# Kernel tuning notes

Hardware: AMD Instinct MI355X
Metric: run time of the kernel (lower is better)

The kernel has to match this reference:

```python
import jax, jax.numpy as jnp
import numpy as np

B, Q, K = 4, 128, 1024
DQ, DK, DV, H = 512, 512, 512, 256
NEG_INF = -1e6


def setup_inputs() -> dict:
    key = jax.random.key(0)
    ks = jax.random.split(key, 6)
    queries = jax.random.normal(ks[0], (B, Q, DQ), dtype=jnp.float32)
    keys = jax.random.normal(ks[1], (B, K, DK), dtype=jnp.float32)
    values = jax.random.normal(ks[2], (B, K, DV), dtype=jnp.float32)
    valid_lens = jax.random.randint(ks[3], (B,), 1, K + 1, dtype=jnp.int32)
    # Learned params (Dense use_bias=False): W_q [DQ,H], W_k [DK,H], w_v [H] (Dense(1) squeezed)
    Wq = jax.random.normal(ks[4], (DQ, H), dtype=jnp.float32) / np.sqrt(DQ)
    Wk = jax.random.normal(ks[5], (DK, H), dtype=jnp.float32) / np.sqrt(DK)
    wv = jax.random.normal(jax.random.fold_in(key, 7), (H,), dtype=jnp.float32) / np.sqrt(H)
    return {"queries": queries, "keys": keys, "values": values,
            "valid_lens": valid_lens, "Wq": Wq, "Wk": Wk, "wv": wv}


def reference(queries, keys, values, valid_lens, Wq, Wk, wv):
    q = queries @ Wq                       # [B,Q,H]
    k = keys @ Wk                          # [B,K,H]
    feats = jnp.tanh(q[:, :, None, :] + k[:, None, :, :])   # [B,Q,K,H]
    scores = jnp.einsum('bqkh,h->bqk', feats, wv)            # [B,Q,K]
    mask = jnp.arange(scores.shape[-1]) < valid_lens[:, None, None]  # [B,1,K]
    scores = jnp.where(mask, scores, NEG_INF)
    attn = jax.nn.softmax(scores, axis=-1)                   # [B,Q,K]
    # dropout is identity at inference
    return attn @ values                                     # [B,Q,DV]
```

## Files before the change

kernel.cpp:

```cpp
#include <hip/hip_runtime.h>

#define Bn 4
#define Qn 128
#define Kn 1024
#define Dn 512
#define Hn 256

__device__ __forceinline__ float fast_tanh(float x) {
    float e = __expf(2.0f * x);
    return 1.0f - 2.0f * __builtin_amdgcn_rcpf(1.0f + e);
}

#define PBK 64

__global__ __launch_bounds__(512, 4) void proj_kernel(
    const float* __restrict__ queries, const float* __restrict__ keys,
    const float* __restrict__ Wq, const float* __restrict__ Wk,
    const int* __restrict__ valid_lens,
    float* __restrict__ proj0, float* __restrict__ proj1)
{
    const int blk = blockIdx.x;
    const int kc = blk & 1;
    const int nt = (blk >> 1) & 3;
    const int mt = blk >> 3;
    const int t = threadIdx.x;
    const float* Asrc; const float* W;
    int m0, drow;
    if (mt < 8) {
        m0 = mt * 64;
        drow = m0;
        Asrc = queries; W = Wq;
    } else {
        int r0 = (mt - 8) * 64;
        int b = r0 >> 10;
        if ((r0 & 1023) >= valid_lens[b]) return;
        m0 = r0;
        drow = 512 + r0;
        Asrc = keys; W = Wk;
    }
    const int n0 = nt * 64;
    const int k0 = kc * 256;
    float* Dst = (kc ? proj1 : proj0) + (size_t)drow * Hn;

    __shared__ float s_a[PBK][68];
    __shared__ float s_b[PBK][64];

    const int tt   = t & 255;
    const int kh   = t >> 8;
    const int trow = tt >> 4;
    const int tcol = tt & 15;
    const int kklo = kh << 5;

    const int lrow = t >> 4;
    const int lc4  = t & 15;

    float acc[4][4] = {{0.f}};
    float4 ra[2], rb[2];

    #pragma unroll
    for (int i = 0; i < 2; ++i) {
        ra[i] = *(const float4*)(Asrc + (size_t)(m0 + lrow + i * 32) * Dn + k0 + lc4 * 4);
        rb[i] = *(const float4*)(W + (size_t)(k0 + lrow + i * 32) * Hn + n0 + lc4 * 4);
    }

    for (int kt = 0; kt < 4; ++kt) {
        __syncthreads();
        #pragma unroll
        for (int i = 0; i < 2; ++i) {
            int row = lrow + i * 32;
            s_a[lc4 * 4 + 0][row] = ra[i].x;
            s_a[lc4 * 4 + 1][row] = ra[i].y;
            s_a[lc4 * 4 + 2][row] = ra[i].z;
            s_a[lc4 * 4 + 3][row] = ra[i].w;
            *(float4*)&s_b[row][lc4 * 4] = rb[i];
        }
        __syncthreads();
        if (kt < 3) {
            const int d0n = k0 + (kt + 1) * PBK;
            #pragma unroll
            for (int i = 0; i < 2; ++i) {
                ra[i] = *(const float4*)(Asrc + (size_t)(m0 + lrow + i * 32) * Dn + d0n + lc4 * 4);
                rb[i] = *(const float4*)(W + (size_t)(d0n + lrow + i * 32) * Hn + n0 + lc4 * 4);
            }
        }
        #pragma unroll
        for (int kk = 0; kk < 32; ++kk) {
            float4 a4 = *(const float4*)&s_a[kklo + kk][trow * 4];
            float4 b4 = *(const float4*)&s_b[kklo + kk][tcol * 4];
            float a[4] = {a4.x, a4.y, a4.z, a4.w};
            float b[4] = {b4.x, b4.y, b4.z, b4.w};
            #pragma unroll
            for (int i = 0; i < 4; ++i)
                #pragma unroll
                for (int j = 0; j < 4; ++j)
                    acc[i][j] += a[i] * b[j];
        }
    }

    __syncthreads();
    float* red = &s_a[0][0];
    if (kh) {
        #pragma unroll
        for (int i = 0; i < 4; ++i)
            #pragma unroll
            for (int j = 0; j < 4; ++j)
                red[tt * 17 + i * 4 + j] = acc[i][j];
    }
    __syncthreads();
    if (!kh) {
        #pragma unroll
        for (int i = 0; i < 4; ++i) {
            float4 o;
            o.x = acc[i][0] + red[tt * 17 + i * 4 + 0];
            o.y = acc[i][1] + red[tt * 17 + i * 4 + 1];
            o.z = acc[i][2] + red[tt * 17 + i * 4 + 2];
            o.w = acc[i][3] + red[tt * 17 + i * 4 + 3];
            *(float4*)(Dst + (size_t)(trow * 4 + i) * Hn + n0 + tcol * 4) = o;
        }
    }
}

#define SK_KT 16
#define SK_PAD 260

__global__ __launch_bounds__(256) void score_kernel(
    const float* __restrict__ proj0, const float* __restrict__ proj1,
    const float* __restrict__ wv, const int* __restrict__ valid_lens,
    float* __restrict__ escores, float* __restrict__ rowsum)
{
    const int blk = blockIdx.x;
    const int kt = blk & 63;
    const int qt = (blk >> 6) & 31;
    const int b  = blk >> 11;
    const int vlen = valid_lens[b];
    const int k0 = kt * SK_KT;
    if (k0 >= vlen) return;
    const int q0 = qt * 4;
    const int t = threadIdx.x;

    __shared__ float s_k[SK_KT * SK_PAD];
    __shared__ float s_q[4 * Hn];
    __shared__ float s_wv[Hn];

    {
        const float4* k0p = reinterpret_cast<const float4*>(
            proj0 + ((size_t)512 + (size_t)b * Kn + k0) * Hn);
        const float4* k1p = reinterpret_cast<const float4*>(
            proj1 + ((size_t)512 + (size_t)b * Kn + k0) * Hn);
        #pragma unroll
        for (int i = 0; i < 4; ++i) {
            int idx = t + i * 256;
            int row = idx >> 6, c4 = idx & 63;
            float4 a = k0p[idx];
            float4 c = k1p[idx];
            a.x += c.x; a.y += c.y; a.z += c.z; a.w += c.w;
            *reinterpret_cast<float4*>(&s_k[row * SK_PAD + c4 * 4]) = a;
        }
        float4 qa = reinterpret_cast<const float4*>(
            proj0 + ((size_t)b * Qn + q0) * Hn)[t];
        float4 qb = reinterpret_cast<const float4*>(
            proj1 + ((size_t)b * Qn + q0) * Hn)[t];
        qa.x += qb.x; qa.y += qb.y; qa.z += qb.z; qa.w += qb.w;
        reinterpret_cast<float4*>(s_q)[t] = qa;
        if (t < 64)
            reinterpret_cast<float4*>(s_wv)[t] =
                reinterpret_cast<const float4*>(wv)[t];
    }
    __syncthreads();

    const int wave = t >> 6;
    const int lane = t & 63;
    const int kloc = lane & 15;
    const int hq   = lane >> 4;

    const float4* kr = reinterpret_cast<const float4*>(&s_k[kloc * SK_PAD + hq * 64]);
    const float4* qr = reinterpret_cast<const float4*>(&s_q[wave * Hn + hq * 64]);
    const float4* wr = reinterpret_cast<const float4*>(&s_wv[hq * 64]);

    float s = 0.0f;
    #pragma unroll
    for (int i = 0; i < 16; ++i) {
        float4 kv = kr[i];
        float4 qv = qr[i];
        float4 wq = wr[i];
        s += wq.x * fast_tanh(qv.x + kv.x);
        s += wq.y * fast_tanh(qv.y + kv.y);
        s += wq.z * fast_tanh(qv.z + kv.z);
        s += wq.w * fast_tanh(qv.w + kv.w);
    }
    s += __shfl_xor(s, 16, 64);
    s += __shfl_xor(s, 32, 64);

    const int k = k0 + kloc;
    float e = 0.0f;
    if (lane < 16 && k < vlen) {
        e = __expf(s);
        escores[((size_t)b * Qn + q0 + wave) * Kn + k] = e;
    }
    #pragma unroll
    for (int off = 32; off; off >>= 1)
        e += __shfl_xor(e, off, 64);
    if (lane == 0)
        atomicAdd(&rowsum[b * Qn + q0 + wave], e);
}

__global__ __launch_bounds__(256) void av_kernel(
    const float* __restrict__ escores, const float* __restrict__ values,
    const float* __restrict__ rowsum, float* __restrict__ out)
{
    const int blk = blockIdx.x;
    const int kc = blk & 3;
    const int dh = (blk >> 2) & 1;
    const int qt = (blk >> 3) & 15;
    const int b  = blk >> 7;
    const int t = threadIdx.x;
    const int q0 = qt * 8;
    const int kb = kc * 256;
    const int d  = dh * 256 + t;

    __shared__ float s_e[8][256];
    #pragma unroll
    for (int i = 0; i < 2; ++i) {
        int idx = t + i * 256;
        int row = idx >> 6, c4 = idx & 63;
        *(float4*)&s_e[row][c4 * 4] = *(const float4*)(
            escores + ((size_t)(b * Qn + q0 + row)) * Kn + kb + c4 * 4);
    }
    __syncthreads();

    const float* vb = values + ((size_t)b * Kn + kb) * Dn + d;
    float acc[8] = {0.f};
    #pragma unroll 2
    for (int k = 0; k < 256; k += 4) {
        float v0 = vb[(size_t)(k + 0) * Dn];
        float v1 = vb[(size_t)(k + 1) * Dn];
        float v2 = vb[(size_t)(k + 2) * Dn];
        float v3 = vb[(size_t)(k + 3) * Dn];
        #pragma unroll
        for (int j = 0; j < 8; ++j) {
            float4 e4 = *(const float4*)&s_e[j][k];
            acc[j] += e4.x * v0 + e4.y * v1 + e4.z * v2 + e4.w * v3;
        }
    }
    float* op = out + ((size_t)(b * Qn + q0)) * Dn + d;
    #pragma unroll
    for (int j = 0; j < 8; ++j) {
        float inv = __builtin_amdgcn_rcpf(rowsum[b * Qn + q0 + j]);
        atomicAdd(op + (size_t)j * Dn, acc[j] * inv);
    }
}

extern "C" void kernel_launch(void* const* d_in, const int* in_sizes, int n_in,
                              void* d_out, int out_size, void* d_ws, size_t ws_size,
                              hipStream_t stream) {
    const float* queries    = (const float*)d_in[0];
    const float* keys       = (const float*)d_in[1];
    const float* values     = (const float*)d_in[2];
    const int*   valid_lens = (const int*)  d_in[3];
    const float* Wq         = (const float*)d_in[4];
    const float* Wk         = (const float*)d_in[5];
    const float* wv         = (const float*)d_in[6];
    float* out = (float*)d_out;

    const size_t PROJ_F = (size_t)4608 * Hn;
    float* proj0   = (float*)d_ws;
    float* proj1   = proj0 + PROJ_F;
    float* escores = proj1 + PROJ_F;
    float* rowsum  = escores + (size_t)Bn * Qn * Kn;

    hipMemsetAsync(escores, 0, (size_t)(Bn * Qn * Kn + Bn * Qn) * sizeof(float),
                   stream);
    hipMemsetAsync(out, 0, (size_t)Bn * Qn * Dn * sizeof(float), stream);
    proj_kernel<<<576, 512, 0, stream>>>(queries, keys, Wq, Wk, valid_lens,
                                         proj0, proj1);
    score_kernel<<<Bn * 32 * 64, 256, 0, stream>>>(proj0, proj1, wv,
                                                   valid_lens, escores, rowsum);
    av_kernel<<<512, 256, 0, stream>>>(escores, values, rowsum, out);
}
```

Before: 153.4 us.

## Fuse projection, scoring and AV into one cooperative persistent kernel

Replaces the three kernels and two memsets with a single cooperative kernel of 256 blocks. Blocks zero the output and rowsum buffers themselves, run the projection GEMM as a loop over jobs, and separate the stages with grid-wide syncs. The score stage is retiled so each wave handles 8 query rows, which reuses each key tile across more queries. The AV stage now skips key chunks past valid_len. This removes launch and memset overhead and raises data reuse. In exchange it runs at lower parallelism (256 blocks), no longer skips projecting masked key rows, and the uneven job split across blocks may leave some blocks idle at each grid sync.

```diff
diff --git a/kernel.cpp b/kernel.cpp
--- a/kernel.cpp
+++ b/kernel.cpp
@@ -1,4 +1,7 @@
 #include <hip/hip_runtime.h>
+#include <hip/hip_cooperative_groups.h>
+
+namespace cg = cooperative_groups;
 
 #define Bn 4
 #define Qn 128
@@ -11,242 +14,238 @@
     return 1.0f - 2.0f * __builtin_amdgcn_rcpf(1.0f + e);
 }
 
-#define PBK 64
-
-__global__ __launch_bounds__(512, 4) void proj_kernel(
+__global__ __launch_bounds__(512) void fused_kernel(
     const float* __restrict__ queries, const float* __restrict__ keys,
+    const float* __restrict__ values, const int* __restrict__ valid_lens,
     const float* __restrict__ Wq, const float* __restrict__ Wk,
-    const int* __restrict__ valid_lens,
-    float* __restrict__ proj0, float* __restrict__ proj1)
+    const float* __restrict__ wv,
+    float* __restrict__ proj0, float* __restrict__ proj1,
+    float* __restrict__ escores, float* __restrict__ rowsum,
+    float* __restrict__ out)
 {
+    __shared__ float smem[20800];
+    const int t = threadIdx.x;
     const int blk = blockIdx.x;
-    const int kc = blk & 1;
-    const int nt = (blk >> 1) & 3;
-    const int mt = blk >> 3;
-    const int t = threadIdx.x;
-    const float* Asrc; const float* W;
-    int m0, drow;
-    if (mt < 8) {
-        m0 = mt * 64;
-        drow = m0;
-        Asrc = queries; W = Wq;
-    } else {
-        int r0 = (mt - 8) * 64;
-        int b = r0 >> 10;
-        if ((r0 & 1023) >= valid_lens[b]) return;
-        m0 = r0;
-        drow = 512 + r0;
-        Asrc = keys; W = Wk;
-    }
-    const int n0 = nt * 64;
-    const int k0 = kc * 256;
-    float* Dst = (kc ? proj1 : proj0) + (size_t)drow * Hn;
-
-    __shared__ float s_a[PBK][68];
-    __shared__ float s_b[PBK][64];
-
-    const int tt   = t & 255;
-    const int kh   = t >> 8;
-    const int trow = tt >> 4;
-    const int tcol = tt & 15;
-    const int kklo = kh << 5;
-
-    const int lrow = t >> 4;
-    const int lc4  = t & 15;
-
-    float acc[4][4] = {{0.f}};
-    float4 ra[2], rb[2];
-
-    #pragma unroll
-    for (int i = 0; i < 2; ++i) {
-        ra[i] = *(const float4*)(Asrc + (size_t)(m0 + lrow + i * 32) * Dn + k0 + lc4 * 4);
-        rb[i] = *(const float4*)(W + (size_t)(k0 + lrow + i * 32) * Hn + n0 + lc4 * 4);
-    }
-
-    for (int kt = 0; kt < 4; ++kt) {
-        __syncthreads();
-        #pragma unroll
-        for (int i = 0; i < 2; ++i) {
-            int row = lrow + i * 32;
-            s_a[lc4 * 4 + 0][row] = ra[i].x;
-            s_a[lc4 * 4 + 1][row] = ra[i].y;
-            s_a[lc4 * 4 + 2][row] = ra[i].z;
-            s_a[lc4 * 4 + 3][row] = ra[i].w;
-            *(float4*)&s_b[row][lc4 * 4] = rb[i];
+    cg::grid_group grid = cg::this_grid();
+
+    {
+        const int gid = blk * 512 + t;
+        float4 z = {0.f, 0.f, 0.f, 0.f};
+        if (gid < (Bn * Qn * Dn) / 4) ((float4*)out)[gid] = z;
+        if (gid < (Bn * Qn) / 4)      ((float4*)rowsum)[gid] = z;
+    }
+
+    {
+        float* s_a = smem;
+        float* s_b = smem + 64 * 68;
+        const int lrow = t >> 4, lc4 = t & 15;
+        const int tt = t & 255, kh = t >> 8;
+        const int trow = tt >> 4, tcol = tt & 15;
+        const int kklo = kh << 5;
+
+        for (int job = blk; job < 576; job += 256) {
+            const int kc = job & 1;
+            const int nt = (job >> 1) & 3;
+            const int mt = job >> 3;
+            const float *Asrc, *W; int m0, drow;
+            if (mt < 8) { m0 = mt * 64;       drow = m0;       Asrc = queries; W = Wq; }
+            else        { m0 = (mt - 8) * 64; drow = 512 + m0; Asrc = keys;    W = Wk; }
+            const int n0 = nt * 64;
+            const int kb = kc * 256;
+            float* Dst = (kc ? proj1 : proj0) + (size_t)drow * Hn;
+
+            float acc[4][4] = {{0.f}};
+            float4 ra[2], rb[2];
+            #pragma unroll
+            for (int i = 0; i < 2; ++i) {
+                ra[i] = *(const float4*)(Asrc + (size_t)(m0 + lrow + i * 32) * Dn + kb + lc4 * 4);
+                rb[i] = *(const float4*)(W + (size_t)(kb + lrow + i * 32) * Hn + n0 + lc4 * 4);
+            }
+            for (int kt = 0; kt < 4; ++kt) {
+                __syncthreads();
+                #pragma unroll
+                for (int i = 0; i < 2; ++i) {
+                    int row = lrow + i * 32;
+                    s_a[(lc4 * 4 + 0) * 68 + row] = ra[i].x;
+                    s_a[(lc4 * 4 + 1) * 68 + row] = ra[i].y;
+                    s_a[(lc4 * 4 + 2) * 68 + row] = ra[i].z;
+                    s_a[(lc4 * 4 + 3) * 68 + row] = ra[i].w;
+                    *(float4*)&s_b[row * 64 + lc4 * 4] = rb[i];
+                }
+                __syncthreads();
+                if (kt < 3) {
+                    const int d0n = kb + (kt + 1) * 64;
+                    #pragma unroll
+                    for (int i = 0; i < 2; ++i) {
+                        ra[i] = *(const float4*)(Asrc + (size_t)(m0 + lrow + i * 32) * Dn + d0n + lc4 * 4);
+                        rb[i] = *(const float4*)(W + (size_t)(d0n + lrow + i * 32) * Hn + n0 + lc4 * 4);
+                    }
+                }
+                #pragma unroll
+                for (int kk = 0; kk < 32; ++kk) {
+                    float4 a4 = *(const float4*)&s_a[(kklo + kk) * 68 + trow * 4];
+                    float4 b4 = *(const float4*)&s_b[(kklo + kk) * 64 + tcol * 4];
+                    float a[4] = {a4.x, a4.y, a4.z, a4.w};
+                    float b[4] = {b4.x, b4.y, b4.z, b4.w};
+                    #pragma unroll
+                    for (int i = 0; i < 4; ++i)
+                        #pragma unroll
+                        for (int j = 0; j < 4; ++j)
+                            acc[i][j] += a[i] * b[j];
+                }
+            }
+            __syncthreads();
+            float* red = smem;
+            if (kh) {
+                #pragma unroll
+                for (int i = 0; i < 4; ++i)
+                    #pragma unroll
+                    for (int j = 0; j < 4; ++j)
+                        red[tt * 17 + i * 4 + j] = acc[i][j];
+            }
+            __syncthreads();
+            if (!kh) {
+                #pragma unroll
+                for (int i = 0; i < 4; ++i) {
+                    float4 o;
+                    o.x = acc[i][0] + red[tt * 17 + i * 4 + 0];
+                    o.y = acc[i][1] + red[tt * 17 + i * 4 + 1];
+                    o.z = acc[i][2] + red[tt * 17 + i * 4 + 2];
+                    o.w = acc[i][3] + red[tt * 17 + i * 4 + 3];
+                    *(float4*)(Dst + (size_t)(trow * 4 + i) * Hn + n0 + tcol * 4) = o;
+                }
+            }
+            __syncthreads();
         }
-        __syncthreads();
-        if (kt < 3) {
-            const int d0n = k0 + (kt + 1) * PBK;
+    }
+
+    __threadfence();
+    grid.sync();
+    __threadfence();
+
+    {
+        float* s_k  = smem;
+        float* s_q  = smem + 16 * 260;
+        float* s_wv = smem + 16 * 260 + 64 * 256;
+        for (int job = blk; job < 512; job += 256) {
+            const int kt = job & 63;
+            const int qh = (job >> 6) & 1;
+            const int b  = job >> 7;
+            const int vlen = valid_lens[b];
+            const int k0 = kt * 16;
+            if (k0 >= vlen) continue;
+            const int q0 = qh * 64;
+
+            const float4* k0p = (const float4*)(proj0 + ((size_t)512 + b * Kn + k0) * Hn);
+            const float4* k1p = (const float4*)(proj1 + ((size_t)512 + b * Kn + k0) * Hn);
             #pragma unroll
             for (int i = 0; i < 2; ++i) {
-                ra[i] = *(const float4*)(Asrc + (size_t)(m0 + lrow + i * 32) * Dn + d0n + lc4 * 4);
-                rb[i] = *(const float4*)(W + (size_t)(d0n + lrow + i * 32) * Hn + n0 + lc4 * 4);
-            }
+                int idx = t + i * 512;
+                int row = idx >> 6, c4 = idx & 63;
+                float4 a = k0p[idx], c = k1p[idx];
+                a.x += c.x; a.y += c.y; a.z += c.z; a.w += c.w;
+                *(float4*)&s_k[row * 260 + c4 * 4] = a;
+            }
+            const float4* q0p = (const float4*)(proj0 + ((size_t)b * Qn + q0) * Hn);
+            const float4* q1p = (const float4*)(proj1 + ((size_t)b * Qn + q0) * Hn);
+            #pragma unroll
+            for (int i = 0; i < 8; ++i) {
+                int idx = t + i * 512;
+                float4 a = q0p[idx], c = q1p[idx];
+                a.x += c.x; a.y += c.y; a.z += c.z; a.w += c.w;
+                ((float4*)s_q)[idx] = a;
+            }
+            if (t < 64) ((float4*)s_wv)[t] = ((const float4*)wv)[t];
+            __syncthreads();
+
+            const int w = t >> 6, lane = t & 63;
+            const int kloc = lane & 15, hq = lane >> 4;
+            const float4* kr = (const float4*)&s_k[kloc * 260 + hq * 64];
+            const float4* wr = (const float4*)&s_wv[hq * 64];
+            const float*  qb = &s_q[(size_t)(w * 8) * 256 + hq * 64];
+            float acc[8] = {0.f, 0.f, 0.f, 0.f, 0.f, 0.f, 0.f, 0.f};
+            #pragma unroll 4
+            for (int i = 0; i < 16; ++i) {
+                float4 kv = kr[i];
+                float4 wq = wr[i];
+                #pragma unroll
+                for (int qr = 0; qr < 8; ++qr) {
+                    float4 qv = *(const float4*)&qb[qr * 256 + i * 4];
+                    acc[qr] += wq.x * fast_tanh(qv.x + kv.x)
+                             + wq.y * fast_tanh(qv.y + kv.y)
+                             + wq.z * fast_tanh(qv.z + kv.z)
+                             + wq.w * fast_tanh(qv.w + kv.w);
+                }
+            }
+            const int k = k0 + kloc;
+            #pragma unroll
+            for (int qr = 0; qr < 8; ++qr) {
+                float s = acc[qr];
+                s += __shfl_xor(s, 16, 64);
+                s += __shfl_xor(s, 32, 64);
+                float e = 0.f;
+                if (lane < 16 && k < vlen) {
+                    e = __expf(s);
+                    escores[((size_t)b * Qn + q0 + w * 8 + qr) * Kn + k] = e;
+                }
+                e += __shfl_xor(e, 8, 64);
+                e += __shfl_xor(e, 4, 64);
+                e += __shfl_xor(e, 2, 64);
+                e += __shfl_xor(e, 1, 64);
+                if (lane == 0)
+                    atomicAdd(&rowsum[b * Qn + q0 + w * 8 + qr], e);
+            }
+            __syncthreads();
         }
-        #pragma unroll
-        for (int kk = 0; kk < 32; ++kk) {
-            float4 a4 = *(const float4*)&s_a[kklo + kk][trow * 4];
-            float4 b4 = *(const float4*)&s_b[kklo + kk][tcol * 4];
-            float a[4] = {a4.x, a4.y, a4.z, a4.w};
-            float b[4] = {b4.x, b4.y, b4.z, b4.w};
-            #pragma unroll
-            for (int i = 0; i < 4; ++i)
-                #pragma unroll
-                for (int j = 0; j < 4; ++j)
-                    acc[i][j] += a[i] * b[j];
+    }
+
+    __threadfence();
+    grid.sync();
+    __threadfence();
+
+    {
+        float* s_e = smem;
+        const int kc = blk & 3;
+        const int qt = (blk >> 2) & 15;
+        const int b  = blk >> 6;
+        const int vlen = valid_lens[b];
+        const int kb = kc * 256;
+        if (kb < vlen) {
+            const int q0 = qt * 8;
+            const int row = t >> 6, c4 = t & 63;
+            {
+                const float* esrc = escores + ((size_t)b * Qn + q0 + row) * Kn + kb + c4 * 4;
+                const int kbase = kb + c4 * 4;
+                float4 ev;
+                ev.x = (kbase + 0 < vlen) ? esrc[0] : 0.f;
+                ev.y = (kbase + 1 < vlen) ? esrc[1] : 0.f;
+                ev.z = (kbase + 2 < vlen) ? esrc[2] : 0.f;
+                ev.w = (kbase + 3 < vlen) ? esrc[3] : 0.f;
+                *(float4*)&s_e[row * 256 + c4 * 4] = ev;
+            }
+            __syncthreads();
+            const int d = t;
+            const float* vb = values + ((size_t)b * Kn + kb) * Dn + d;
+            float acc[8] = {0.f, 0.f, 0.f, 0.f, 0.f, 0.f, 0.f, 0.f};
+            #pragma unroll 2
+            for (int k = 0; k < 256; k += 4) {
+                float v0 = vb[(size_t)(k + 0) * Dn];
+                float v1 = vb[(size_t)(k + 1) * Dn];
+                float v2 = vb[(size_t)(k + 2) * Dn];
+                float v3 = vb[(size_t)(k + 3) * Dn];
+                #pragma unroll
+                for (int j = 0; j < 8; ++j) {
+                    float4 e4 = *(const float4*)&s_e[j * 256 + k];
+                    acc[j] += e4.x * v0 + e4.y * v1 + e4.z * v2 + e4.w * v3;
+                }
+            }
+            float* op = out + ((size_t)b * Qn + q0) * Dn + d;
+            #pragma unroll
+            for (int j = 0; j < 8; ++j) {
+                float inv = __builtin_amdgcn_rcpf(rowsum[b * Qn + q0 + j]);
+                atomicAdd(op + (size_t)j * Dn, acc[j] * inv);
+            }
         }
-    }
-
-    __syncthreads();
-    float* red = &s_a[0][0];
-    if (kh) {
-        #pragma unroll
-        for (int i = 0; i < 4; ++i)
-            #pragma unroll
-            for (int j = 0; j < 4; ++j)
-                red[tt * 17 + i * 4 + j] = acc[i][j];
-    }
-    __syncthreads();
-    if (!kh) {
-        #pragma unroll
-        for (int i = 0; i < 4; ++i) {
-            float4 o;
-            o.x = acc[i][0] + red[tt * 17 + i * 4 + 0];
-            o.y = acc[i][1] + red[tt * 17 + i * 4 + 1];
-            o.z = acc[i][2] + red[tt * 17 + i * 4 + 2];
-            o.w = acc[i][3] + red[tt * 17 + i * 4 + 3];
-            *(float4*)(Dst + (size_t)(trow * 4 + i) * Hn + n0 + tcol * 4) = o;
-        }
-    }
-}
-
-#define SK_KT 16
-#define SK_PAD 260
-
-__global__ __launch_bounds__(256) void score_kernel(
-    const float* __restrict__ proj0, const float* __restrict__ proj1,
-    const float* __restrict__ wv, const int* __restrict__ valid_lens,
-    float* __restrict__ escores, float* __restrict__ rowsum)
-{
-    const int blk = blockIdx.x;
-    const int kt = blk & 63;
-    const int qt = (blk >> 6) & 31;
-    const int b  = blk >> 11;
-    const int vlen = valid_lens[b];
-    const int k0 = kt * SK_KT;
-    if (k0 >= vlen) return;
-    const int q0 = qt * 4;
-    const int t = threadIdx.x;
-
-    __shared__ float s_k[SK_KT * SK_PAD];
-    __shared__ float s_q[4 * Hn];
-    __shared__ float s_wv[Hn];
-
-    {
-        const float4* k0p = reinterpret_cast<const float4*>(
-            proj0 + ((size_t)512 + (size_t)b * Kn + k0) * Hn);
-        const float4* k1p = reinterpret_cast<const float4*>(
-            proj1 + ((size_t)512 + (size_t)b * Kn + k0) * Hn);
-        #pragma unroll
-        for (int i = 0; i < 4; ++i) {
-            int idx = t + i * 256;
-            int row = idx >> 6, c4 = idx & 63;
-            float4 a = k0p[idx];
-            float4 c = k1p[idx];
-            a.x += c.x; a.y += c.y; a.z += c.z; a.w += c.w;
-            *reinterpret_cast<float4*>(&s_k[row * SK_PAD + c4 * 4]) = a;
-        }
-        float4 qa = reinterpret_cast<const float4*>(
-            proj0 + ((size_t)b * Qn + q0) * Hn)[t];
-        float4 qb = reinterpret_cast<const float4*>(
-            proj1 + ((size_t)b * Qn + q0) * Hn)[t];
-        qa.x += qb.x; qa.y += qb.y; qa.z += qb.z; qa.w += qb.w;
-        reinterpret_cast<float4*>(s_q)[t] = qa;
-        if (t < 64)
-            reinterpret_cast<float4*>(s_wv)[t] =
-                reinterpret_cast<const float4*>(wv)[t];
-    }
-    __syncthreads();
-
-    const int wave = t >> 6;
-    const int lane = t & 63;
-    const int kloc = lane & 15;
-    const int hq   = lane >> 4;
-
-    const float4* kr = reinterpret_cast<const float4*>(&s_k[kloc * SK_PAD + hq * 64]);
-    const float4* qr = reinterpret_cast<const float4*>(&s_q[wave * Hn + hq * 64]);
-    const float4* wr = reinterpret_cast<const float4*>(&s_wv[hq * 64]);
-
-    float s = 0.0f;
-    #pragma unroll
-    for (int i = 0; i < 16; ++i) {
-        float4 kv = kr[i];
-        float4 qv = qr[i];
-        float4 wq = wr[i];
-        s += wq.x * fast_tanh(qv.x + kv.x);
-        s += wq.y * fast_tanh(qv.y + kv.y);
-        s += wq.z * fast_tanh(qv.z + kv.z);
-        s += wq.w * fast_tanh(qv.w + kv.w);
-    }
-    s += __shfl_xor(s, 16, 64);
-    s += __shfl_xor(s, 32, 64);
-
-    const int k = k0 + kloc;
-    float e = 0.0f;
-    if (lane < 16 && k < vlen) {
-        e = __expf(s);
-        escores[((size_t)b * Qn + q0 + wave) * Kn + k] = e;
-    }
-    #pragma unroll
-    for (int off = 32; off; off >>= 1)
-        e += __shfl_xor(e, off, 64);
-    if (lane == 0)
-        atomicAdd(&rowsum[b * Qn + q0 + wave], e);
-}
-
-__global__ __launch_bounds__(256) void av_kernel(
-    const float* __restrict__ escores, const float* __restrict__ values,
-    const float* __restrict__ rowsum, float* __restrict__ out)
-{
-    const int blk = blockIdx.x;
-    const int kc = blk & 3;
-    const int dh = (blk >> 2) & 1;
-    const int qt = (blk >> 3) & 15;
-    const int b  = blk >> 7;
-    const int t = threadIdx.x;
-    const int q0 = qt * 8;
-    const int kb = kc * 256;
-    const int d  = dh * 256 + t;
-
-    __shared__ float s_e[8][256];
-    #pragma unroll
-    for (int i = 0; i < 2; ++i) {
-        int idx = t + i * 256;
-        int row = idx >> 6, c4 = idx & 63;
-        *(float4*)&s_e[row][c4 * 4] = *(const float4*)(
-            escores + ((size_t)(b * Qn + q0 + row)) * Kn + kb + c4 * 4);
-    }
-    __syncthreads();
-
-    const float* vb = values + ((size_t)b * Kn + kb) * Dn + d;
-    float acc[8] = {0.f};
-    #pragma unroll 2
-    for (int k = 0; k < 256; k += 4) {
-        float v0 = vb[(size_t)(k + 0) * Dn];
-        float v1 = vb[(size_t)(k + 1) * Dn];
-        float v2 = vb[(size_t)(k + 2) * Dn];
-        float v3 = vb[(size_t)(k + 3) * Dn];
-        #pragma unroll
-        for (int j = 0; j < 8; ++j) {
-            float4 e4 = *(const float4*)&s_e[j][k];
-            acc[j] += e4.x * v0 + e4.y * v1 + e4.z * v2 + e4.w * v3;
-        }
-    }
-    float* op = out + ((size_t)(b * Qn + q0)) * Dn + d;
-    #pragma unroll
-    for (int j = 0; j < 8; ++j) {
-        float inv = __builtin_amdgcn_rcpf(rowsum[b * Qn + q0 + j]);
-        atomicAdd(op + (size_t)j * Dn, acc[j] * inv);
     }
 }
 
@@ -268,12 +267,10 @@
     float* escores = proj1 + PROJ_F;
     float* rowsum  = escores + (size_t)Bn * Qn * Kn;
 
-    hipMemsetAsync(escores, 0, (size_t)(Bn * Qn * Kn + Bn * Qn) * sizeof(float),
-                   stream);
-    hipMemsetAsync(out, 0, (size_t)Bn * Qn * Dn * sizeof(float), stream);
-    proj_kernel<<<576, 512, 0, stream>>>(queries, keys, Wq, Wk, valid_lens,
-                                         proj0, proj1);
-    score_kernel<<<Bn * 32 * 64, 256, 0, stream>>>(proj0, proj1, wv,
-                                                   valid_lens, escores, rowsum);
-    av_kernel<<<512, 256, 0, stream>>>(escores, values, rowsum, out);
+    void* args[] = {(void*)&queries, (void*)&keys, (void*)&values,
+                    (void*)&valid_lens, (void*)&Wq, (void*)&Wk, (void*)&wv,
+                    (void*)&proj0, (void*)&proj1, (void*)&escores,
+                    (void*)&rowsum, (void*)&out};
+    hipLaunchCooperativeKernel(fused_kernel, dim3(256), dim3(512),
+                               args, 0u, stream);
 }
```

New measurement: 381.8 us. +148.9%, slower.
